# Optimization experiments

Hardware: AMD Instinct MI355X
Metric: run time of the kernel (lower is better)

Reference implementation:

```python
import jax, jax.numpy as jnp
import numpy as np

D = 256   # state.D, per-node vector width
B = 16    # batch
L = 8     # depth layers (hidden), all < t_budget
N = 128   # nodes per depth layer
LAMBDA_ASYNC = 0.08
LAMBDA_TAU = 0.12
BOOST_SCALE = 1.0


def setup_inputs() -> dict:
    key = jax.random.key(0)
    ks = jax.random.split(key, 6)
    X = jax.random.normal(ks[0], (B, D), jnp.float32)
    # per-node weight matrices, scaled so tanh stays in linear-ish regime
    W = jax.random.normal(ks[1], (L, N, D, D), jnp.float32) / np.sqrt(D).astype(np.float32)
    bias = jax.random.normal(ks[2], (L, N, D), jnp.float32) * 0.01
    S = jax.random.normal(ks[3], (L, N, D), jnp.float32) / np.sqrt(D).astype(np.float32)
    rho = jax.random.uniform(ks[4], (L, N), jnp.float32, minval=0.2, maxval=0.6)
    boost = jax.random.normal(ks[5], (L, N), jnp.float32) * 0.01  # residue.decode(node_id)
    return {"X": X, "W": W, "bias": bias, "S": S, "rho": rho, "boost": boost, "t_budget": 15}


def reference(X, W, bias, S, rho, boost, t_budget):
    # Messages routed at depth d are consumed at depth d+1 -> decay = exp(-lambda_async * 1)
    decay = jnp.exp(jnp.float32(-LAMBDA_ASYNC))
    tb = jnp.float32(t_budget)

    def step(carry, layer):
        V_in, has_input = carry            # V_in: (B, D) aggregated inbox, shared under dense routing
        Wl, bl, Sl, rl, gl, depth = layer  # (N,D,D), (N,D), (N,D), (N,), (N,), scalar
        # anytime threshold tau(t) = 0.5 * exp(lambda_tau * (t - t_budget))
        tau = 0.5 * jnp.exp(LAMBDA_TAU * (depth - tb))
        # s_dot.mean(): mean over batch of <V_in, S_n>, per node -> (N,)
        s_dot = jnp.einsum('bd,nd->n', V_in, Sl) / jnp.float32(B)
        rho_active = rl + s_dot + gl * BOOST_SCALE
        fired = (rho_active >= tau) & has_input                      # (N,) thresholded firing
        # V_weighted = apply_W_batch(V_in) + bias, per node
        V_w = jnp.einsum('bd,nde->nbe', V_in, Wl) + bl[:, None, :]   # (N, B, D)
        V_out = jnp.tanh(V_w)                                        # pointwise primitive
        fmask = fired.astype(V_out.dtype)
        cnt = jnp.maximum(fmask.sum(), jnp.float32(1.0))
        # inbox aggregation at next depth: decayed mean over fired contributors
        V_next = decay * jnp.einsum('n,nbe->be', fmask, V_out) / cnt
        return (V_next, fmask.sum() > 0), (V_out, fired)

    depths = jnp.arange(1, L + 1, dtype=jnp.float32)
    (_, _), (V_all, fired_all) = jax.lax.scan(
        step, (X, jnp.array(True)), (W, bias, S, rho, boost, depths))
    # output = mean over fired output-layer (last depth) nodes
    last_V, last_f = V_all[-1], fired_all[-1]
    fm = last_f.astype(last_V.dtype)
    out = jnp.einsum('n,nbe->be', fm, last_V) / jnp.maximum(fm.sum(), jnp.float32(1.0))
    return out
```

## Files before the change

kernel.cpp:

```cpp
#include <hip/hip_runtime.h>
#include <math.h>

#define D 256
#define B 16
#define L 8
#define N 128

static constexpr float LAMBDA_ASYNC = 0.08f;
static constexpr float LAMBDA_TAU   = 0.12f;


#define OFF_COLSUM 4096
#define OFF_META   4352
#define OFF_FIRED  4368
#define OFF_SLAB   4496

__global__ __launch_bounds__(256) void transpose_kernel(
    const float* __restrict__ X, float* __restrict__ xt,
    float* __restrict__ colsum) {
    const int d = threadIdx.x;
    float cs = 0.0f;
    #pragma unroll
    for (int b = 0; b < B; ++b) {
        const float v = X[b * D + d];
        xt[d * 16 + b] = v;
        cs += v;
    }
    colsum[d] = cs;
}

__global__ __launch_bounds__(256) void layer_kernel(
    const float* __restrict__ Wl,
    const float* __restrict__ biasl,
    const float* __restrict__ Sl,
    const float* __restrict__ rhol,
    const float* __restrict__ boostl,
    const int*  __restrict__ tb,
    const float* __restrict__ vin_src,
    const float* __restrict__ colsum,
    const float* __restrict__ meta_prev,
    float* __restrict__ slab,
    float* __restrict__ fired_cur,
    float depth, int is_first)
{
    __shared__ float vin[D * 16];
    __shared__ float red[4 * 64 * 17];
    __shared__ float sh[4];

    const int t    = threadIdx.x;
    const int w    = t >> 6;
    const int lane = t & 63;
    const int n    = blockIdx.x >> 2;
    const int e0   = (blockIdx.x & 3) * 64;

    const float* wp = Wl + ((size_t)n * D + (size_t)(w * 64)) * D + (e0 + lane);
    float wa[8], wb[8];
    #pragma unroll
    for (int i = 0; i < 8; ++i) wa[i] = wp[(size_t)i * D];

    float part = colsum[t] * Sl[n * D + t];
    #pragma unroll
    for (int o = 32; o > 0; o >>= 1) part += __shfl_down(part, o);
    if (lane == 0) sh[w] = part;
    __syncthreads();
    {
        const bool has_input = is_first ? true : (meta_prev[0] > 0.0f);
        const float sdot = (sh[0] + sh[1] + sh[2] + sh[3]) * (1.0f / 16.0f);
        const float tau  = 0.5f * expf(LAMBDA_TAU * (depth - (float)tb[0]));
        const bool fired = (rhol[n] + sdot + boostl[n] >= tau) && has_input;
        if (e0 == 0 && t == 0) fired_cur[n] = fired ? 1.0f : 0.0f;
        if (!fired) return;
    }

    {
        const float4* s4 = (const float4*)vin_src;
        #pragma unroll
        for (int k = 0; k < 4; ++k)
            ((float4*)vin)[t * 4 + k] = s4[t * 4 + k];
    }
    __syncthreads();

    const int dbase = w * 64;
    float acc[16];
    #pragma unroll
    for (int b = 0; b < 16; ++b) acc[b] = 0.0f;

    #pragma unroll
    for (int c = 0; c < 8; ++c) {
        float* cur = (c & 1) ? wb : wa;
        float* nxt = (c & 1) ? wa : wb;
        if (c < 7) {
            #pragma unroll
            for (int i = 0; i < 8; ++i)
                nxt[i] = wp[(size_t)((c + 1) * 8 + i) * D];
        }
        #pragma unroll
        for (int i = 0; i < 8; ++i) {
            const float* vr = &vin[(dbase + c * 8 + i) * 16];
            const float4 v0 = *(const float4*)(vr + 0);
            const float4 v1 = *(const float4*)(vr + 4);
            const float4 v2 = *(const float4*)(vr + 8);
            const float4 v3 = *(const float4*)(vr + 12);
            const float wj = cur[i];
            acc[ 0] = fmaf(wj, v0.x, acc[ 0]);
            acc[ 1] = fmaf(wj, v0.y, acc[ 1]);
            acc[ 2] = fmaf(wj, v0.z, acc[ 2]);
            acc[ 3] = fmaf(wj, v0.w, acc[ 3]);
            acc[ 4] = fmaf(wj, v1.x, acc[ 4]);
            acc[ 5] = fmaf(wj, v1.y, acc[ 5]);
            acc[ 6] = fmaf(wj, v1.z, acc[ 6]);
            acc[ 7] = fmaf(wj, v1.w, acc[ 7]);
            acc[ 8] = fmaf(wj, v2.x, acc[ 8]);
            acc[ 9] = fmaf(wj, v2.y, acc[ 9]);
            acc[10] = fmaf(wj, v2.z, acc[10]);
            acc[11] = fmaf(wj, v2.w, acc[11]);
            acc[12] = fmaf(wj, v3.x, acc[12]);
            acc[13] = fmaf(wj, v3.y, acc[13]);
            acc[14] = fmaf(wj, v3.z, acc[14]);
            acc[15] = fmaf(wj, v3.w, acc[15]);
        }
    }

    {
        float* rr = &red[(w * 64 + lane) * 17];
        #pragma unroll
        for (int b = 0; b < 16; ++b) rr[b] = acc[b];
    }
    __syncthreads();

    {
        const int e_loc = t >> 2;
        const int b0    = (t & 3) * 4;
        const float bv  = biasl[n * D + e0 + e_loc];
        float4 o4;
        float s[4];
        #pragma unroll
        for (int q = 0; q < 4; ++q) {
            const int b = b0 + q;
            s[q] = red[(0 * 64 + e_loc) * 17 + b]
                 + red[(1 * 64 + e_loc) * 17 + b]
                 + red[(2 * 64 + e_loc) * 17 + b]
                 + red[(3 * 64 + e_loc) * 17 + b];
        }
        o4.x = tanhf(s[0] + bv);
        o4.y = tanhf(s[1] + bv);
        o4.z = tanhf(s[2] + bv);
        o4.w = tanhf(s[3] + bv);
        *(float4*)(slab + (size_t)n * 4096 + (size_t)(e0 + e_loc) * 16 + b0) = o4;
    }
}

__global__ __launch_bounds__(256) void reduce_mid(
    const float* __restrict__ slab, const float* __restrict__ fired_l,
    float* __restrict__ acct, float* __restrict__ colsum,
    float* __restrict__ meta)
{
    __shared__ float part[256];
    __shared__ float shcnt;
    const int t    = threadIdx.x;
    const int cell = blockIdx.x * 64 + (t & 63);
    const int n0   = (t >> 6) * 32;

    float s = 0.0f;
    #pragma unroll 8
    for (int k = 0; k < 32; ++k)
        s = fmaf(fired_l[n0 + k], slab[(size_t)(n0 + k) * 4096 + cell], s);
    part[t] = s;

    if (t < 64) {
        float c = fired_l[t] + fired_l[t + 64];
        #pragma unroll
        for (int o = 32; o > 0; o >>= 1) c += __shfl_down(c, o);
        if (t == 0) shcnt = c;
    }
    __syncthreads();

    if (t < 64) {
        const float cnt   = shcnt;
        const float scale = expf(-LAMBDA_ASYNC) / fmaxf(cnt, 1.0f);
        float v = (part[t] + part[64 + t] + part[128 + t] + part[192 + t]) * scale;
        acct[blockIdx.x * 64 + t] = v;
        float cs = v;
        cs += __shfl_down(cs, 8);
        cs += __shfl_down(cs, 4);
        cs += __shfl_down(cs, 2);
        cs += __shfl_down(cs, 1);
        if ((t & 15) == 0) colsum[(blockIdx.x * 64 + t) >> 4] = cs;
        if (blockIdx.x == 0 && t == 0) meta[0] = cnt;
    }
}

__global__ __launch_bounds__(256) void reduce_final(
    const float* __restrict__ slab, const float* __restrict__ fired_l,
    float* __restrict__ out)
{
    __shared__ float part[256];
    __shared__ float shcnt;
    const int t    = threadIdx.x;
    const int cell = blockIdx.x * 64 + (t & 63);
    const int n0   = (t >> 6) * 32;

    float s = 0.0f;
    #pragma unroll 8
    for (int k = 0; k < 32; ++k)
        s = fmaf(fired_l[n0 + k], slab[(size_t)(n0 + k) * 4096 + cell], s);
    part[t] = s;

    if (t < 64) {
        float c = fired_l[t] + fired_l[t + 64];
        #pragma unroll
        for (int o = 32; o > 0; o >>= 1) c += __shfl_down(c, o);
        if (t == 0) shcnt = c;
    }
    __syncthreads();

    if (t < 64) {
        const float inv = 1.0f / fmaxf(shcnt, 1.0f);
        const int c = blockIdx.x * 64 + t;
        const float v = (part[t] + part[64 + t] + part[128 + t] + part[192 + t]) * inv;
        const int e = c >> 4, b = c & 15;
        out[b * 256 + e] = v;
    }
}

extern "C" void kernel_launch(void* const* d_in, const int* in_sizes, int n_in,
                              void* d_out, int out_size, void* d_ws, size_t ws_size,
                              hipStream_t stream)
{
    const float* X     = (const float*)d_in[0];
    const float* W     = (const float*)d_in[1];
    const float* bias  = (const float*)d_in[2];
    const float* S     = (const float*)d_in[3];
    const float* rho   = (const float*)d_in[4];
    const float* boost = (const float*)d_in[5];
    const int*   tb    = (const int*)d_in[6];
    float* out = (float*)d_out;
    float* ws  = (float*)d_ws;

    float* acct   = ws;
    float* colsum = ws + OFF_COLSUM;
    float* meta   = ws + OFF_META;
    float* fired  = ws + OFF_FIRED;
    float* slab   = ws + OFF_SLAB;

    transpose_kernel<<<dim3(1), dim3(256), 0, stream>>>(X, acct, colsum);

    for (int l = 0; l < L; ++l) {
        layer_kernel<<<dim3(512), dim3(256), 0, stream>>>(
            W + (size_t)l * N * D * D,
            bias + (size_t)l * N * D,
            S + (size_t)l * N * D,
            rho + (size_t)l * N,
            boost + (size_t)l * N,
            tb,
            acct,
            colsum,
            (l == 0) ? (const float*)nullptr : meta,
            slab,
            fired,
            (float)(l + 1), (l == 0) ? 1 : 0);
        if (l < L - 1) {
            reduce_mid<<<dim3(64), dim3(256), 0, stream>>>(
                slab, fired, acct, colsum, meta);
        } else {
            reduce_final<<<dim3(64), dim3(256), 0, stream>>>(
                slab, fired, out);
        }
    }
}
```

Baseline: 119.3 us.

## Split layer GEMV over input-dim chunks with float4 weight loads, defer tanh to reduce

Each layer block now owns a node and a slice of the input dimension instead of a slice of output columns. Each thread loads float4 weight rows covering 4 output columns, so weight reads are wider and coalesced. Blocks write raw partial sums into a larger slab, and the reduce kernel sums the NQ partials, adds bias, applies tanh and skips non-fired nodes. This trades more slab traffic and tanh work in the reduce step for better weight streaming, with NQ chosen from the available workspace size.

```diff
diff --git a/kernel.cpp b/kernel.cpp
--- a/kernel.cpp
+++ b/kernel.cpp
@@ -14,6 +14,12 @@
 #define OFF_META   4352
 #define OFF_FIRED  4368
 #define OFF_SLAB   4496
+
+__device__ __forceinline__ float4 fma4(float s, float4 w, float4 a) {
+    a.x = fmaf(s, w.x, a.x); a.y = fmaf(s, w.y, a.y);
+    a.z = fmaf(s, w.z, a.z); a.w = fmaf(s, w.w, a.w);
+    return a;
+}
 
 __global__ __launch_bounds__(256) void transpose_kernel(
     const float* __restrict__ X, float* __restrict__ xt,
@@ -29,9 +35,9 @@
     colsum[d] = cs;
 }
 
-__global__ __launch_bounds__(256) void layer_kernel(
+template<int NQ>
+__global__ __launch_bounds__(256, 4) void layer_kernel(
     const float* __restrict__ Wl,
-    const float* __restrict__ biasl,
     const float* __restrict__ Sl,
     const float* __restrict__ rhol,
     const float* __restrict__ boostl,
@@ -41,22 +47,20 @@
     const float* __restrict__ meta_prev,
     float* __restrict__ slab,
     float* __restrict__ fired_cur,
-    float depth, int is_first)
-{
-    __shared__ float vin[D * 16];
-    __shared__ float red[4 * 64 * 17];
+    float depth)
+{
+    constexpr int DR = 256 / NQ;
+    constexpr int WR = DR / 4;
+
+    __shared__ float vin[DR * 16];
+    __shared__ float red[2][16][256];
     __shared__ float sh[4];
 
     const int t    = threadIdx.x;
     const int w    = t >> 6;
     const int lane = t & 63;
-    const int n    = blockIdx.x >> 2;
-    const int e0   = (blockIdx.x & 3) * 64;
-
-    const float* wp = Wl + ((size_t)n * D + (size_t)(w * 64)) * D + (e0 + lane);
-    float wa[8], wb[8];
-    #pragma unroll
-    for (int i = 0; i < 8; ++i) wa[i] = wp[(size_t)i * D];
+    const int n    = blockIdx.x / NQ;
+    const int q    = blockIdx.x - n * NQ;
 
     float part = colsum[t] * Sl[n * D + t];
     #pragma unroll
@@ -64,107 +68,125 @@
     if (lane == 0) sh[w] = part;
     __syncthreads();
     {
-        const bool has_input = is_first ? true : (meta_prev[0] > 0.0f);
+        const bool has_input = (meta_prev == nullptr) ? true : (meta_prev[0] > 0.0f);
         const float sdot = (sh[0] + sh[1] + sh[2] + sh[3]) * (1.0f / 16.0f);
         const float tau  = 0.5f * expf(LAMBDA_TAU * (depth - (float)tb[0]));
         const bool fired = (rhol[n] + sdot + boostl[n] >= tau) && has_input;
-        if (e0 == 0 && t == 0) fired_cur[n] = fired ? 1.0f : 0.0f;
+        if (q == 0 && t == 0) fired_cur[n] = fired ? 1.0f : 0.0f;
         if (!fired) return;
     }
 
     {
-        const float4* s4 = (const float4*)vin_src;
-        #pragma unroll
-        for (int k = 0; k < 4; ++k)
-            ((float4*)vin)[t * 4 + k] = s4[t * 4 + k];
-    }
-    __syncthreads();
-
-    const int dbase = w * 64;
-    float acc[16];
-    #pragma unroll
-    for (int b = 0; b < 16; ++b) acc[b] = 0.0f;
-
-    #pragma unroll
-    for (int c = 0; c < 8; ++c) {
-        float* cur = (c & 1) ? wb : wa;
-        float* nxt = (c & 1) ? wa : wb;
-        if (c < 7) {
-            #pragma unroll
-            for (int i = 0; i < 8; ++i)
-                nxt[i] = wp[(size_t)((c + 1) * 8 + i) * D];
-        }
-        #pragma unroll
-        for (int i = 0; i < 8; ++i) {
-            const float* vr = &vin[(dbase + c * 8 + i) * 16];
-            const float4 v0 = *(const float4*)(vr + 0);
-            const float4 v1 = *(const float4*)(vr + 4);
-            const float4 v2 = *(const float4*)(vr + 8);
-            const float4 v3 = *(const float4*)(vr + 12);
-            const float wj = cur[i];
-            acc[ 0] = fmaf(wj, v0.x, acc[ 0]);
-            acc[ 1] = fmaf(wj, v0.y, acc[ 1]);
-            acc[ 2] = fmaf(wj, v0.z, acc[ 2]);
-            acc[ 3] = fmaf(wj, v0.w, acc[ 3]);
-            acc[ 4] = fmaf(wj, v1.x, acc[ 4]);
-            acc[ 5] = fmaf(wj, v1.y, acc[ 5]);
-            acc[ 6] = fmaf(wj, v1.z, acc[ 6]);
-            acc[ 7] = fmaf(wj, v1.w, acc[ 7]);
-            acc[ 8] = fmaf(wj, v2.x, acc[ 8]);
-            acc[ 9] = fmaf(wj, v2.y, acc[ 9]);
-            acc[10] = fmaf(wj, v2.z, acc[10]);
-            acc[11] = fmaf(wj, v2.w, acc[11]);
-            acc[12] = fmaf(wj, v3.x, acc[12]);
-            acc[13] = fmaf(wj, v3.y, acc[13]);
-            acc[14] = fmaf(wj, v3.z, acc[14]);
-            acc[15] = fmaf(wj, v3.w, acc[15]);
-        }
-    }
+        const float4* s4 = (const float4*)(vin_src + q * DR * 16);
+        #pragma unroll
+        for (int k = 0; k < DR / 64; ++k)
+            ((float4*)vin)[t + k * 256] = s4[t + k * 256];
+    }
+    __syncthreads();
+
+    const int d0 = q * DR + w * WR;
+    const float* wp = Wl + ((size_t)n * D + (size_t)d0) * D + 4 * lane;
+
+    float4 accv[16];
+    #pragma unroll
+    for (int b = 0; b < 16; ++b) accv[b] = make_float4(0.f, 0.f, 0.f, 0.f);
+
+    float4 wbuf[2][2];
+    wbuf[0][0] = *(const float4*)(wp + (size_t)0 * D);
+    wbuf[0][1] = *(const float4*)(wp + (size_t)1 * D);
+
+    #pragma unroll
+    for (int c = 0; c < WR / 2; ++c) {
+        const int pb = c & 1, nb = pb ^ 1;
+        if (c < WR / 2 - 1) {
+            wbuf[nb][0] = *(const float4*)(wp + (size_t)(2 * c + 2) * D);
+            wbuf[nb][1] = *(const float4*)(wp + (size_t)(2 * c + 3) * D);
+        }
+        #pragma unroll
+        for (int r = 0; r < 2; ++r) {
+            const float* vr = &vin[(w * WR + 2 * c + r) * 16];
+            const float4 vA = *(const float4*)(vr + 0);
+            const float4 vB = *(const float4*)(vr + 4);
+            const float4 vC = *(const float4*)(vr + 8);
+            const float4 vD = *(const float4*)(vr + 12);
+            const float4 wv = wbuf[pb][r];
+            accv[ 0] = fma4(vA.x, wv, accv[ 0]);
+            accv[ 1] = fma4(vA.y, wv, accv[ 1]);
+            accv[ 2] = fma4(vA.z, wv, accv[ 2]);
+            accv[ 3] = fma4(vA.w, wv, accv[ 3]);
+            accv[ 4] = fma4(vB.x, wv, accv[ 4]);
+            accv[ 5] = fma4(vB.y, wv, accv[ 5]);
+            accv[ 6] = fma4(vB.z, wv, accv[ 6]);
+            accv[ 7] = fma4(vB.w, wv, accv[ 7]);
+            accv[ 8] = fma4(vC.x, wv, accv[ 8]);
+            accv[ 9] = fma4(vC.y, wv, accv[ 9]);
+            accv[10] = fma4(vC.z, wv, accv[10]);
+            accv[11] = fma4(vC.w, wv, accv[11]);
+            accv[12] = fma4(vD.x, wv, accv[12]);
+            accv[13] = fma4(vD.y, wv, accv[13]);
+            accv[14] = fma4(vD.z, wv, accv[14]);
+            accv[15] = fma4(vD.w, wv, accv[15]);
+        }
+    }
+
+    if (w >= 2) {
+        #pragma unroll
+        for (int b = 0; b < 16; ++b)
+            *(float4*)&red[w - 2][b][4 * lane] = accv[b];
+    }
+    __syncthreads();
+    if (w < 2) {
+        #pragma unroll
+        for (int b = 0; b < 16; ++b) {
+            float4 o = *(const float4*)&red[w][b][4 * lane];
+            o.x += accv[b].x; o.y += accv[b].y;
+            o.z += accv[b].z; o.w += accv[b].w;
+            *(float4*)&red[w][b][4 * lane] = o;
+        }
+    }
+    __syncthreads();
 
     {
-        float* rr = &red[(w * 64 + lane) * 17];
-        #pragma unroll
-        for (int b = 0; b < 16; ++b) rr[b] = acc[b];
-    }
-    __syncthreads();
-
-    {
-        const int e_loc = t >> 2;
-        const int b0    = (t & 3) * 4;
-        const float bv  = biasl[n * D + e0 + e_loc];
-        float4 o4;
-        float s[4];
-        #pragma unroll
-        for (int q = 0; q < 4; ++q) {
-            const int b = b0 + q;
-            s[q] = red[(0 * 64 + e_loc) * 17 + b]
-                 + red[(1 * 64 + e_loc) * 17 + b]
-                 + red[(2 * 64 + e_loc) * 17 + b]
-                 + red[(3 * 64 + e_loc) * 17 + b];
-        }
-        o4.x = tanhf(s[0] + bv);
-        o4.y = tanhf(s[1] + bv);
-        o4.z = tanhf(s[2] + bv);
-        o4.w = tanhf(s[3] + bv);
-        *(float4*)(slab + (size_t)n * 4096 + (size_t)(e0 + e_loc) * 16 + b0) = o4;
-    }
-}
-
-__global__ __launch_bounds__(256) void reduce_mid(
-    const float* __restrict__ slab, const float* __restrict__ fired_l,
+        const int e = t;
+        float* dst = slab + ((size_t)(n * NQ + q)) * 4096 + (size_t)e * 16;
+        #pragma unroll
+        for (int b4 = 0; b4 < 4; ++b4) {
+            float4 o;
+            o.x = red[0][b4 * 4 + 0][e] + red[1][b4 * 4 + 0][e];
+            o.y = red[0][b4 * 4 + 1][e] + red[1][b4 * 4 + 1][e];
+            o.z = red[0][b4 * 4 + 2][e] + red[1][b4 * 4 + 2][e];
+            o.w = red[0][b4 * 4 + 3][e] + red[1][b4 * 4 + 3][e];
+            *(float4*)(dst + b4 * 4) = o;
+        }
+    }
+}
+
+template<int NQ, bool IS_FINAL>
+__global__ __launch_bounds__(256) void reduce_kernel(
+    const float* __restrict__ slab, const float* __restrict__ biasl,
+    const float* __restrict__ fired_l,
     float* __restrict__ acct, float* __restrict__ colsum,
-    float* __restrict__ meta)
+    float* __restrict__ meta, float* __restrict__ out)
 {
     __shared__ float part[256];
     __shared__ float shcnt;
     const int t    = threadIdx.x;
     const int cell = blockIdx.x * 64 + (t & 63);
     const int n0   = (t >> 6) * 32;
+    const int e    = cell >> 4;
 
     float s = 0.0f;
-    #pragma unroll 8
-    for (int k = 0; k < 32; ++k)
-        s = fmaf(fired_l[n0 + k], slab[(size_t)(n0 + k) * 4096 + cell], s);
+    for (int k = 0; k < 32; ++k) {
+        const int n = n0 + k;
+        const float f = fired_l[n];
+        if (f > 0.0f) {
+            float p = 0.0f;
+            #pragma unroll
+            for (int qq = 0; qq < NQ; ++qq)
+                p += slab[((size_t)(n * NQ + qq)) * 4096 + cell];
+            s += tanhf(p + biasl[n * D + e]);
+        }
+    }
     part[t] = s;
 
     if (t < 64) {
@@ -176,50 +198,59 @@
     __syncthreads();
 
     if (t < 64) {
-        const float cnt   = shcnt;
-        const float scale = expf(-LAMBDA_ASYNC) / fmaxf(cnt, 1.0f);
-        float v = (part[t] + part[64 + t] + part[128 + t] + part[192 + t]) * scale;
-        acct[blockIdx.x * 64 + t] = v;
-        float cs = v;
-        cs += __shfl_down(cs, 8);
-        cs += __shfl_down(cs, 4);
-        cs += __shfl_down(cs, 2);
-        cs += __shfl_down(cs, 1);
-        if ((t & 15) == 0) colsum[(blockIdx.x * 64 + t) >> 4] = cs;
-        if (blockIdx.x == 0 && t == 0) meta[0] = cnt;
-    }
-}
-
-__global__ __launch_bounds__(256) void reduce_final(
-    const float* __restrict__ slab, const float* __restrict__ fired_l,
-    float* __restrict__ out)
-{
-    __shared__ float part[256];
-    __shared__ float shcnt;
-    const int t    = threadIdx.x;
-    const int cell = blockIdx.x * 64 + (t & 63);
-    const int n0   = (t >> 6) * 32;
-
-    float s = 0.0f;
-    #pragma unroll 8
-    for (int k = 0; k < 32; ++k)
-        s = fmaf(fired_l[n0 + k], slab[(size_t)(n0 + k) * 4096 + cell], s);
-    part[t] = s;
-
-    if (t < 64) {
-        float c = fired_l[t] + fired_l[t + 64];
-        #pragma unroll
-        for (int o = 32; o > 0; o >>= 1) c += __shfl_down(c, o);
-        if (t == 0) shcnt = c;
-    }
-    __syncthreads();
-
-    if (t < 64) {
-        const float inv = 1.0f / fmaxf(shcnt, 1.0f);
+        const float cnt = shcnt;
         const int c = blockIdx.x * 64 + t;
-        const float v = (part[t] + part[64 + t] + part[128 + t] + part[192 + t]) * inv;
-        const int e = c >> 4, b = c & 15;
-        out[b * 256 + e] = v;
+        const float tot = part[t] + part[64 + t] + part[128 + t] + part[192 + t];
+        if (IS_FINAL) {
+            const float v = tot / fmaxf(cnt, 1.0f);
+            out[(c & 15) * 256 + (c >> 4)] = v;
+        } else {
+            const float scale = expf(-LAMBDA_ASYNC) / fmaxf(cnt, 1.0f);
+            const float v = tot * scale;
+            acct[c] = v;
+            float cs = v;
+            cs += __shfl_down(cs, 8);
+            cs += __shfl_down(cs, 4);
+            cs += __shfl_down(cs, 2);
+            cs += __shfl_down(cs, 1);
+            if ((t & 15) == 0) colsum[c >> 4] = cs;
+            if (blockIdx.x == 0 && t == 0) meta[0] = cnt;
+        }
+    }
+}
+
+template<int NQ>
+static void run_pipeline(const float* X, const float* W, const float* bias,
+                         const float* S, const float* rho, const float* boost,
+                         const int* tb, float* out, float* ws, hipStream_t stream)
+{
+    float* acct   = ws;
+    float* colsum = ws + OFF_COLSUM;
+    float* meta   = ws + OFF_META;
+    float* fired  = ws + OFF_FIRED;
+    float* slab   = ws + OFF_SLAB;
+
+    transpose_kernel<<<dim3(1), dim3(256), 0, stream>>>(X, acct, colsum);
+
+    for (int l = 0; l < L; ++l) {
+        layer_kernel<NQ><<<dim3(N * NQ), dim3(256), 0, stream>>>(
+            W + (size_t)l * N * D * D,
+            S + (size_t)l * N * D,
+            rho + (size_t)l * N,
+            boost + (size_t)l * N,
+            tb,
+            acct, colsum,
+            (l == 0) ? (const float*)nullptr : meta,
+            slab, fired, (float)(l + 1));
+        if (l < L - 1) {
+            reduce_kernel<NQ, false><<<dim3(64), dim3(256), 0, stream>>>(
+                slab, bias + (size_t)l * N * D, fired,
+                acct, colsum, meta, out);
+        } else {
+            reduce_kernel<NQ, true><<<dim3(64), dim3(256), 0, stream>>>(
+                slab, bias + (size_t)l * N * D, fired,
+                acct, colsum, meta, out);
+        }
     }
 }
 
@@ -237,34 +268,13 @@
     float* out = (float*)d_out;
     float* ws  = (float*)d_ws;
 
-    float* acct   = ws;
-    float* colsum = ws + OFF_COLSUM;
-    float* meta   = ws + OFF_META;
-    float* fired  = ws + OFF_FIRED;
-    float* slab   = ws + OFF_SLAB;
-
-    transpose_kernel<<<dim3(1), dim3(256), 0, stream>>>(X, acct, colsum);
-
-    for (int l = 0; l < L; ++l) {
-        layer_kernel<<<dim3(512), dim3(256), 0, stream>>>(
-            W + (size_t)l * N * D * D,
-            bias + (size_t)l * N * D,
-            S + (size_t)l * N * D,
-            rho + (size_t)l * N,
-            boost + (size_t)l * N,
-            tb,
-            acct,
-            colsum,
-            (l == 0) ? (const float*)nullptr : meta,
-            slab,
-            fired,
-            (float)(l + 1), (l == 0) ? 1 : 0);
-        if (l < L - 1) {
-            reduce_mid<<<dim3(64), dim3(256), 0, stream>>>(
-                slab, fired, acct, colsum, meta);
-        } else {
-            reduce_final<<<dim3(64), dim3(256), 0, stream>>>(
-                slab, fired, out);
-        }
-    }
-}
+    const size_t need4 = (size_t)(OFF_SLAB + N * 4 * 4096) * sizeof(float);
+    const size_t need2 = (size_t)(OFF_SLAB + N * 2 * 4096) * sizeof(float);
+
+    if (ws_size >= need4)
+        run_pipeline<4>(X, W, bias, S, rho, boost, tb, out, ws, stream);
+    else if (ws_size >= need2)
+        run_pipeline<2>(X, W, bias, S, rho, boost, tb, out, ws, stream);
+    else
+        run_pipeline<1>(X, W, bias, S, rho, boost, tb, out, ws, stream);
+}
```

Result: slower. 298.2 us (+150.1%).
